# Kernel tuning notes

Hardware: AMD Instinct MI355X
Metric: run time of the kernel (lower is better)

The kernel has to match this reference:

```python
import jax, jax.numpy as jnp
import numpy as np

DIM = 1024
N_HEADS = 16
HEAD_DIM = DIM // N_HEADS


def setup_inputs() -> dict:
    key = jax.random.key(0)
    ks = jax.random.split(key, 5)
    s = 0.02
    return {
        "x": jax.random.normal(ks[0], (2, 2048, DIM), dtype=jnp.float32),
        "w_qkv": jax.random.normal(ks[1], (DIM, 3 * DIM), dtype=jnp.float32) * s,
        "b_qkv": jnp.zeros((3 * DIM,), dtype=jnp.float32),
        "w_proj": jax.random.normal(ks[2], (DIM, DIM), dtype=jnp.float32) * s,
        "b_proj": jnp.zeros((DIM,), dtype=jnp.float32),
    }


def reference(x, w_qkv, b_qkv, w_proj, b_proj):
    B, N, C = x.shape
    H, D = N_HEADS, HEAD_DIM
    qkv = x @ w_qkv + b_qkv                      # [B, N, 3C]
    qkv = qkv.reshape(B, N, 3, H, D)
    q = qkv[:, :, 0].transpose(0, 2, 1, 3)       # [B, H, N, D]
    k = qkv[:, :, 1].transpose(0, 2, 1, 3)
    v = qkv[:, :, 2].transpose(0, 2, 1, 3)
    scale = 1.0 / np.sqrt(D).astype(np.float32)
    attn = jnp.einsum('bhnd,bhmd->bhnm', q, k) * scale
    attn = jax.nn.softmax(attn, axis=-1)
    out = jnp.einsum('bhnm,bhmd->bhnd', attn, v)  # [B, H, N, D]
    out = out.transpose(0, 2, 1, 3).reshape(B, N, C)
    return out @ w_proj + b_proj
```

## Files before the change

### kernel.cpp

```cpp
#include <hip/hip_runtime.h>

#define DIM    1024
#define NHEADS 16
#define HDIM   64
#define BATCH  2
#define SEQ    2048
#define ROWS   (BATCH * SEQ)
#define KDIM   1024

typedef __attribute__((ext_vector_type(4))) float f32x4;
typedef __attribute__((ext_vector_type(16))) float f32x16;
typedef __attribute__((ext_vector_type(8))) short bf16x8;

__device__ inline unsigned short f2bf(float f) {
  return (unsigned short)((__float_as_uint(f) + 0x8000u) >> 16);
}
__device__ inline float bf2f(unsigned short h) {
  return __uint_as_float(((unsigned int)h) << 16);
}
__device__ inline void split2(float x, unsigned short& hi, unsigned short& lo) {
  hi = f2bf(x);
  lo = f2bf(x - bf2f(hi));
}
__device__ inline int key2(int r) { return (r & 3) ^ ((r >> 2) & 3); }
__device__ inline int key8(int r) { return (r & 7) ^ ((r >> 3) & 7); }

__device__ inline void gll16(const void* g, void* lds_base) {
  __builtin_amdgcn_global_load_lds(
      (const __attribute__((address_space(1))) void*)g,
      (__attribute__((address_space(3))) void*)lds_base, 16, 0, 0);
}
__device__ inline unsigned int cvtpk_bf16(float a, float b) {
  unsigned int r;
  asm("v_cvt_pk_bf16_f32 %0, %1, %2" : "=v"(r) : "v"(a), "v"(b));
  return r;
}

__global__ __launch_bounds__(256) void split_x_kernel(
    const float* __restrict__ x, ushort* __restrict__ Xh,
    ushort* __restrict__ Xl) {
  const int i = blockIdx.x * 256 + threadIdx.x;
  const float4 v = ((const float4*)x)[i];
  ushort4 h4, l4;
  split2(v.x, h4.x, l4.x);
  split2(v.y, h4.y, l4.y);
  split2(v.z, h4.z, l4.z);
  split2(v.w, h4.w, l4.w);
  ((ushort4*)Xh)[i] = h4;
  ((ushort4*)Xl)[i] = l4;
}

template <int Ndim, bool LO>
__global__ __launch_bounds__(256) void tsplit_w(const float* __restrict__ W,
                                                ushort* __restrict__ WTh,
                                                ushort* __restrict__ WTl) {
  __shared__ float Ls[64][68];
  const int t = threadIdx.x;
  const int n0 = blockIdx.x * 64, k0 = blockIdx.y * 64;
#pragma unroll
  for (int pass = 0; pass < 4; ++pass) {
    const int kk = pass * 16 + (t >> 4);
    const float4 v =
        *(const float4*)(W + (size_t)(k0 + kk) * Ndim + n0 + (t & 15) * 4);
    *(float4*)&Ls[kk][(t & 15) * 4] = v;
  }
  __syncthreads();
  const int nloc = t >> 2, kc = (t & 3) * 16;
#pragma unroll
  for (int j = 0; j < 4; ++j) {
    ushort4 h4, l4;
    split2(Ls[kc + j * 4 + 0][nloc], h4.x, l4.x);
    split2(Ls[kc + j * 4 + 1][nloc], h4.y, l4.y);
    split2(Ls[kc + j * 4 + 2][nloc], h4.z, l4.z);
    split2(Ls[kc + j * 4 + 3][nloc], h4.w, l4.w);
    const size_t off = (size_t)(n0 + nloc) * KDIM + k0 + kc + j * 4;
    *(ushort4*)(WTh + off) = h4;
    if (LO) *(ushort4*)(WTl + off) = l4;
  }
}

template <int NPROD, int MODE>
__global__ __launch_bounds__(256) void gemm_mfma(
    const ushort* __restrict__ Ahp, const ushort* __restrict__ Alp,
    const ushort* __restrict__ Bhp, const ushort* __restrict__ Blp,
    const float* __restrict__ bias, float* __restrict__ Cout,
    ushort* __restrict__ Qh, ushort* __restrict__ Kh,
    ushort* __restrict__ VTh, int Ndim) {
  constexpr int NPLANES = (NPROD == 3) ? 4 : 3;
  constexpr int CALLS = NPLANES * 512 / 256;
  __shared__ ushort lds[2][NPLANES * 128 * 32];

  const int t = threadIdx.x, w = t >> 6, lane = t & 63;
  const int l15 = lane & 15, lg = lane >> 4;
  const int n0 = blockIdx.x * 128, m0 = blockIdx.y * 128;
  const int wr = (w >> 1) * 64;
  const int wc = (w & 1) * 64;

  const ushort* srcs[4];
  srcs[0] = Ahp + (size_t)m0 * KDIM;
  srcs[1] = Alp + (size_t)m0 * KDIM;
  srcs[2] = Bhp + (size_t)n0 * KDIM;
  srcs[3] = (NPROD == 3) ? (Blp + (size_t)n0 * KDIM) : Bhp;

  f32x4 acc[4][4];
#pragma unroll
  for (int a = 0; a < 4; ++a)
#pragma unroll
    for (int bq = 0; bq < 4; ++bq) acc[a][bq] = (f32x4){0.f, 0.f, 0.f, 0.f};

  auto stage = [&](int bi, int k0) {
#pragma unroll
    for (int i = 0; i < CALLS; ++i) {
      const int cbase = (w * CALLS + i) * 64;
      const int c = cbase + lane;
      const int p = c >> 9, cc = c & 511, r = cc >> 2, s = cc & 3;
      const ushort* g = srcs[p] + (size_t)r * KDIM + k0 + ((s ^ key2(r)) << 3);
      gll16(g, (char*)&lds[bi][0] + cbase * 16);
    }
  };

  stage(0, 0);
  __syncthreads();

  for (int k0 = 0, it = 0; k0 < KDIM; k0 += 32, ++it) {
    const int cur = it & 1;
    if (k0 + 32 < KDIM) stage(cur ^ 1, k0 + 32);
    const ushort* L = &lds[cur][0];

    bf16x8 af[4][2];
#pragma unroll
    for (int mt = 0; mt < 4; ++mt) {
      const int row = wr + mt * 16 + l15;
      const int off = row * 32 + ((lg ^ key2(row)) << 3);
      af[mt][0] = *(const bf16x8*)&L[off];
      af[mt][1] = *(const bf16x8*)&L[4096 + off];
    }
#pragma unroll
    for (int nt = 0; nt < 4; ++nt) {
      const int row = wc + nt * 16 + l15;
      const int off = row * 32 + ((lg ^ key2(row)) << 3);
      const bf16x8 bh_ = *(const bf16x8*)&L[8192 + off];
#pragma unroll
      for (int mt = 0; mt < 4; ++mt) {
        acc[mt][nt] = __builtin_amdgcn_mfma_f32_16x16x32_bf16(
            af[mt][0], bh_, acc[mt][nt], 0, 0, 0);
        acc[mt][nt] = __builtin_amdgcn_mfma_f32_16x16x32_bf16(
            af[mt][1], bh_, acc[mt][nt], 0, 0, 0);
      }
      if constexpr (NPROD == 3) {
        const bf16x8 bl_ = *(const bf16x8*)&L[12288 + off];
#pragma unroll
        for (int mt = 0; mt < 4; ++mt)
          acc[mt][nt] = __builtin_amdgcn_mfma_f32_16x16x32_bf16(
              af[mt][0], bl_, acc[mt][nt], 0, 0, 0);
      }
    }
    __syncthreads();
  }

  if constexpr (MODE == 0) {
#pragma unroll
    for (int nt = 0; nt < 4; ++nt) {
      const int col = n0 + wc + nt * 16 + l15;
      const float bv = bias[col];
#pragma unroll
      for (int mt = 0; mt < 4; ++mt) {
        const int row = m0 + wr + mt * 16 + lg * 4;
#pragma unroll
        for (int r = 0; r < 4; ++r)
          Cout[(size_t)(row + r) * Ndim + col] = acc[mt][nt][r] + bv;
      }
    }
  } else {
    const int sec = n0 >> 10;
#pragma unroll
    for (int nt = 0; nt < 4; ++nt) {
      const int col = n0 + wc + nt * 16 + l15;
      const float bv = bias[col];
      const int cw = col & 1023;
      if (sec == 0) {
#pragma unroll
        for (int mt = 0; mt < 4; ++mt) {
          const int row = m0 + wr + mt * 16 + lg * 4;
#pragma unroll
          for (int r = 0; r < 4; ++r)
            Qh[(size_t)(row + r) * DIM + cw] =
                f2bf((acc[mt][nt][r] + bv) * 0.125f);
        }
      } else if (sec == 1) {
#pragma unroll
        for (int mt = 0; mt < 4; ++mt) {
          const int row = m0 + wr + mt * 16 + lg * 4;
#pragma unroll
          for (int r = 0; r < 4; ++r)
            Kh[(size_t)(row + r) * DIM + cw] = f2bf(acc[mt][nt][r] + bv);
        }
      } else {
        const int h = cw >> 6, d = cw & 63;
#pragma unroll
        for (int mt = 0; mt < 4; ++mt) {
          const int grow = m0 + wr + mt * 16 + lg * 4;
          const int b = grow >> 11, n = grow & 2047;
          ushort4 v4;
          v4.x = f2bf(acc[mt][nt][0] + bv);
          v4.y = f2bf(acc[mt][nt][1] + bv);
          v4.z = f2bf(acc[mt][nt][2] + bv);
          v4.w = f2bf(acc[mt][nt][3] + bv);
          *(ushort4*)(VTh + ((size_t)(b * NHEADS + h) * HDIM + d) * SEQ + n) =
              v4;
        }
      }
    }
  }
}

__global__ __launch_bounds__(256) void attn_mfma32(
    const ushort* __restrict__ Qhp, const ushort* __restrict__ Khp,
    const ushort* __restrict__ VThp, ushort* __restrict__ AOh,
    ushort* __restrict__ AOl) {
  __shared__ ushort KV2[2][2 * 64 * 64];

  const int t = threadIdx.x, w = t >> 6, lane = t & 63;
  const int l31 = lane & 31, hi = lane >> 5;
  const int q0 = blockIdx.x * 128;
  const int bh = blockIdx.y, b = bh >> 4, h = bh & 15;

  bf16x8 qf[4];
  {
    const ushort* qp = Qhp +
        (size_t)(b * SEQ + q0 + w * 32 + l31) * DIM + h * HDIM + hi * 8;
#pragma unroll
    for (int j = 0; j < 4; ++j) qf[j] = *(const bf16x8*)(qp + 16 * j);
  }
  const ushort* kbase = Khp + (size_t)(b * SEQ) * DIM + h * HDIM;
  const ushort* vbase = VThp + (size_t)(b * NHEADS + h) * HDIM * SEQ;

  float l_lane = 0.f;
  f32x16 o_[2];
  o_[0] = f32x16{};
  o_[1] = f32x16{};

  auto stage = [&](int bi, int kt) {
    const int kv0 = kt * 64;
#pragma unroll
    for (int i = 0; i < 4; ++i) {
      const int cbase = (w * 4 + i) * 64;
      const int c = cbase + lane;
      const int p_ = c >> 9, cc = c & 511, r = cc >> 3, s = cc & 7;
      const ushort* g =
          (p_ == 0)
              ? kbase + (size_t)(kv0 + r) * DIM + ((s ^ key8(r)) << 3)
              : vbase + (size_t)r * SEQ + kv0 + ((s ^ key8(r)) << 3);
      gll16(g, (char*)&KV2[bi][0] + cbase * 16);
    }
  };

  constexpr int NT = SEQ / 64;
  stage(0, 0);
  __syncthreads();

  for (int kt = 0; kt < NT; ++kt) {
    const int cur = kt & 1;
    if (kt + 1 < NT) stage(cur ^ 1, kt + 1);

    const ushort* Kt = &KV2[cur][0];
    const ushort* Vt = &KV2[cur][4096];

    f32x16 st[2];
    st[0] = f32x16{};
    st[1] = f32x16{};
#pragma unroll
    for (int j = 0; j < 4; ++j) {
#pragma unroll
      for (int rb = 0; rb < 2; ++rb) {
        const int n = rb * 32 + l31;
        const bf16x8 kf =
            *(const bf16x8*)&Kt[n * 64 + (((2 * j + hi) ^ key8(n)) << 3)];
        st[rb] = __builtin_amdgcn_mfma_f32_32x32x16_bf16(kf, qf[j], st[rb],
                                                         0, 0, 0);
      }
    }

    unsigned int u[2][8];
#pragma unroll
    for (int rb = 0; rb < 2; ++rb) {
      float p[16];
#pragma unroll
      for (int r = 0; r < 16; ++r) {
        p[r] = __expf(st[rb][r]);
        l_lane += p[r];
      }
#pragma unroll
      for (int j = 0; j < 8; ++j) u[rb][j] = cvtpk_bf16(p[2 * j], p[2 * j + 1]);
    }

#pragma unroll
    for (int kc = 0; kc < 4; ++kc) {
      bf16x8 pa;
      {
        const unsigned int* ub = &u[kc >> 1][4 * (kc & 1)];
        unsigned int tmp[4] = {ub[0], ub[1], ub[2], ub[3]};
        pa = *(const bf16x8*)tmp;
      }
#pragma unroll
      for (int dblk = 0; dblk < 2; ++dblk) {
        const int d = dblk * 32 + l31;
        const int rowoff = d * 64;
        const ushort4 va = *(const ushort4*)&Vt[rowoff +
            (((2 * kc) ^ key8(d)) << 3) + 4 * hi];
        const ushort4 vb = *(const ushort4*)&Vt[rowoff +
            (((2 * kc + 1) ^ key8(d)) << 3) + 4 * hi];
        ushort tmp[8] = {va.x, va.y, va.z, va.w, vb.x, vb.y, vb.z, vb.w};
        const bf16x8 vf = *(const bf16x8*)tmp;
        o_[dblk] = __builtin_amdgcn_mfma_f32_32x32x16_bf16(pa, vf, o_[dblk],
                                                           0, 0, 0);
      }
    }
    __syncthreads();
  }

  l_lane += __shfl_xor(l_lane, 32);

  float inv[16];
#pragma unroll
  for (int r = 0; r < 16; ++r) {
    const int ql = (r & 3) + 8 * (r >> 2) + 4 * hi;
    inv[r] = 1.0f / __shfl(l_lane, ql);
  }

#pragma unroll
  for (int dblk = 0; dblk < 2; ++dblk)
#pragma unroll
    for (int r = 0; r < 16; ++r) {
      const int q = q0 + w * 32 + (r & 3) + 8 * (r >> 2) + 4 * hi;
      unsigned short hi16, lo16;
      split2(o_[dblk][r] * inv[r], hi16, lo16);
      const size_t off =
          (size_t)(b * SEQ + q) * DIM + h * HDIM + dblk * 32 + l31;
      AOh[off] = hi16;
      AOl[off] = lo16;
    }
}

extern "C" void kernel_launch(void* const* d_in, const int* in_sizes, int n_in,
                              void* d_out, int out_size, void* d_ws,
                              size_t ws_size, hipStream_t stream) {
  const float* x      = (const float*)d_in[0];
  const float* w_qkv  = (const float*)d_in[1];
  const float* b_qkv  = (const float*)d_in[2];
  const float* w_proj = (const float*)d_in[3];
  const float* b_proj = (const float*)d_in[4];
  float* out = (float*)d_out;

  ushort* p = (ushort*)d_ws;
  ushort* WqT_h = p;  p += (size_t)3072 * 1024;
  ushort* WpT_h = p;  p += (size_t)1024 * 1024;
  ushort* WpT_l = p;  p += (size_t)1024 * 1024;
  ushort* Xh    = p;  p += (size_t)ROWS * 1024;
  ushort* Xl    = p;  p += (size_t)ROWS * 1024;
  ushort* Qh    = p;  p += (size_t)ROWS * 1024;
  ushort* Kh    = p;  p += (size_t)ROWS * 1024;
  ushort* VTh   = p;  p += (size_t)ROWS * 1024;
  ushort* AOh = Xh;
  ushort* AOl = Xl;

  split_x_kernel<<<ROWS * DIM / 4 / 256, 256, 0, stream>>>(x, Xh, Xl);
  tsplit_w<3072, false>
      <<<dim3(48, 16), 256, 0, stream>>>(w_qkv, WqT_h, nullptr);
  tsplit_w<1024, true>
      <<<dim3(16, 16), 256, 0, stream>>>(w_proj, WpT_h, WpT_l);

  gemm_mfma<2, 1><<<dim3(24, 32), 256, 0, stream>>>(
      Xh, Xl, WqT_h, nullptr, b_qkv, nullptr, Qh, Kh, VTh, 3072);

  attn_mfma32<<<dim3(SEQ / 128, BATCH * NHEADS), 256, 0, stream>>>(
      Qh, Kh, VTh, AOh, AOl);

  gemm_mfma<3, 0><<<dim3(8, 32), 256, 0, stream>>>(
      AOh, AOl, WpT_h, WpT_l, b_proj, out, nullptr, nullptr, nullptr, 1024);
}
```

Before: 161.4 us.

## Triple-buffer LDS staging in QKV GEMM and attention with vmcnt-based waits

Moves the QKV GEMM and the attention kernel from double to triple LDS buffering. Each iteration now waits on a partial vmcnt count and issues one raw barrier instead of a full __syncthreads at both ends, so global-to-LDS loads run two tiles ahead of compute. It also raises wave priority around the MFMA sections and forces the Q register loads to complete early. The cost is more LDS per block, which may lower occupancy, and correctness now depends on the hand-coded vmcnt values matching the number of loads issued per stage.

```diff
diff --git a/kernel.cpp b/kernel.cpp
--- a/kernel.cpp
+++ b/kernel.cpp
@@ -34,6 +34,13 @@
   unsigned int r;
   asm("v_cvt_pk_bf16_f32 %0, %1, %2" : "=v"(r) : "v"(a), "v"(b));
   return r;
+}
+template <int N>
+__device__ inline void vm_wait() {
+  if constexpr (N == 0)      asm volatile("s_waitcnt vmcnt(0)" ::: "memory");
+  else if constexpr (N == 4) asm volatile("s_waitcnt vmcnt(4)" ::: "memory");
+  else if constexpr (N == 6) asm volatile("s_waitcnt vmcnt(6)" ::: "memory");
+  else                       asm volatile("s_waitcnt vmcnt(8)" ::: "memory");
 }
 
 __global__ __launch_bounds__(256) void split_x_kernel(
@@ -79,7 +86,7 @@
   }
 }
 
-template <int NPROD, int MODE>
+template <int NPROD, int MODE, bool PIPE3>
 __global__ __launch_bounds__(256) void gemm_mfma(
     const ushort* __restrict__ Ahp, const ushort* __restrict__ Alp,
     const ushort* __restrict__ Bhp, const ushort* __restrict__ Blp,
@@ -87,8 +94,10 @@
     ushort* __restrict__ Qh, ushort* __restrict__ Kh,
     ushort* __restrict__ VTh, int Ndim) {
   constexpr int NPLANES = (NPROD == 3) ? 4 : 3;
-  constexpr int CALLS = NPLANES * 512 / 256;
-  __shared__ ushort lds[2][NPLANES * 128 * 32];
+  constexpr int CALLS = NPLANES * 2;
+  constexpr int BUFE = NPLANES * 128 * 32;
+  constexpr int NBUF = PIPE3 ? 3 : 2;
+  __shared__ ushort lds[NBUF][BUFE];
 
   const int t = threadIdx.x, w = t >> 6, lane = t & 63;
   const int l15 = lane & 15, lg = lane >> 4;
@@ -119,14 +128,7 @@
     }
   };
 
-  stage(0, 0);
-  __syncthreads();
-
-  for (int k0 = 0, it = 0; k0 < KDIM; k0 += 32, ++it) {
-    const int cur = it & 1;
-    if (k0 + 32 < KDIM) stage(cur ^ 1, k0 + 32);
-    const ushort* L = &lds[cur][0];
-
+  auto compute = [&](const ushort* L) {
     bf16x8 af[4][2];
 #pragma unroll
     for (int mt = 0; mt < 4; ++mt) {
@@ -135,6 +137,7 @@
       af[mt][0] = *(const bf16x8*)&L[off];
       af[mt][1] = *(const bf16x8*)&L[4096 + off];
     }
+    __builtin_amdgcn_s_setprio(1);
 #pragma unroll
     for (int nt = 0; nt < 4; ++nt) {
       const int row = wc + nt * 16 + l15;
@@ -155,7 +158,29 @@
               af[mt][0], bl_, acc[mt][nt], 0, 0, 0);
       }
     }
+    __builtin_amdgcn_s_setprio(0);
+  };
+
+  if constexpr (PIPE3) {
+    constexpr int NSTEP = KDIM / 32;
+    stage(0, 0);
+    stage(1, 32);
+    for (int it = 0; it < NSTEP; ++it) {
+      if (it + 1 < NSTEP) vm_wait<CALLS>(); else vm_wait<0>();
+      __builtin_amdgcn_s_barrier();
+      __builtin_amdgcn_sched_barrier(0);
+      if (it + 2 < NSTEP) stage((it + 2) % 3, (it + 2) * 32);
+      compute(&lds[it % 3][0]);
+    }
+  } else {
+    stage(0, 0);
     __syncthreads();
+    for (int k0 = 0, it = 0; k0 < KDIM; k0 += 32, ++it) {
+      const int cur = it & 1;
+      if (k0 + 32 < KDIM) stage(cur ^ 1, k0 + 32);
+      compute(&lds[cur][0]);
+      __syncthreads();
+    }
   }
 
   if constexpr (MODE == 0) {
@@ -218,7 +243,7 @@
     const ushort* __restrict__ Qhp, const ushort* __restrict__ Khp,
     const ushort* __restrict__ VThp, ushort* __restrict__ AOh,
     ushort* __restrict__ AOl) {
-  __shared__ ushort KV2[2][2 * 64 * 64];
+  __shared__ ushort KV2[3][2 * 64 * 64];
 
   const int t = threadIdx.x, w = t >> 6, lane = t & 63;
   const int l31 = lane & 31, hi = lane >> 5;
@@ -229,8 +254,15 @@
   {
     const ushort* qp = Qhp +
         (size_t)(b * SEQ + q0 + w * 32 + l31) * DIM + h * HDIM + hi * 8;
-#pragma unroll
-    for (int j = 0; j < 4; ++j) qf[j] = *(const bf16x8*)(qp + 16 * j);
+    int4 qi[4];
+#pragma unroll
+    for (int j = 0; j < 4; ++j) qi[j] = *(const int4*)(qp + 16 * j);
+#pragma unroll
+    for (int j = 0; j < 4; ++j) {
+      asm volatile("" :: "v"(qi[j].x), "v"(qi[j].y), "v"(qi[j].z),
+                   "v"(qi[j].w));
+      qf[j] = __builtin_bit_cast(bf16x8, qi[j]);
+    }
   }
   const ushort* kbase = Khp + (size_t)(b * SEQ) * DIM + h * HDIM;
   const ushort* vbase = VThp + (size_t)(b * NHEADS + h) * HDIM * SEQ;
@@ -257,18 +289,21 @@
 
   constexpr int NT = SEQ / 64;
   stage(0, 0);
-  __syncthreads();
+  stage(1, 1);
 
   for (int kt = 0; kt < NT; ++kt) {
-    const int cur = kt & 1;
-    if (kt + 1 < NT) stage(cur ^ 1, kt + 1);
-
-    const ushort* Kt = &KV2[cur][0];
-    const ushort* Vt = &KV2[cur][4096];
+    if (kt + 1 < NT) vm_wait<4>(); else vm_wait<0>();
+    __builtin_amdgcn_s_barrier();
+    __builtin_amdgcn_sched_barrier(0);
+    if (kt + 2 < NT) stage((kt + 2) % 3, kt + 2);
+
+    const ushort* Kt = &KV2[kt % 3][0];
+    const ushort* Vt = &KV2[kt % 3][4096];
 
     f32x16 st[2];
     st[0] = f32x16{};
     st[1] = f32x16{};
+    __builtin_amdgcn_s_setprio(1);
 #pragma unroll
     for (int j = 0; j < 4; ++j) {
 #pragma unroll
@@ -280,6 +315,7 @@
                                                          0, 0, 0);
       }
     }
+    __builtin_amdgcn_s_setprio(0);
 
     unsigned int u[2][8];
 #pragma unroll
@@ -294,6 +330,7 @@
       for (int j = 0; j < 8; ++j) u[rb][j] = cvtpk_bf16(p[2 * j], p[2 * j + 1]);
     }
 
+    __builtin_amdgcn_s_setprio(1);
 #pragma unroll
     for (int kc = 0; kc < 4; ++kc) {
       bf16x8 pa;
@@ -316,7 +353,7 @@
                                                            0, 0, 0);
       }
     }
-    __syncthreads();
+    __builtin_amdgcn_s_setprio(0);
   }
 
   l_lane += __shfl_xor(l_lane, 32);
@@ -370,12 +407,12 @@
   tsplit_w<1024, true>
       <<<dim3(16, 16), 256, 0, stream>>>(w_proj, WpT_h, WpT_l);
 
-  gemm_mfma<2, 1><<<dim3(24, 32), 256, 0, stream>>>(
+  gemm_mfma<2, 1, true><<<dim3(24, 32), 256, 0, stream>>>(
       Xh, Xl, WqT_h, nullptr, b_qkv, nullptr, Qh, Kh, VTh, 3072);
 
   attn_mfma32<<<dim3(SEQ / 128, BATCH * NHEADS), 256, 0, stream>>>(
       Qh, Kh, VTh, AOh, AOl);
 
-  gemm_mfma<3, 0><<<dim3(8, 32), 256, 0, stream>>>(
+  gemm_mfma<3, 0, false><<<dim3(8, 32), 256, 0, stream>>>(
       AOh, AOl, WpT_h, WpT_l, b_proj, out, nullptr, nullptr, nullptr, 1024);
 }
```

New measurement: 164.9 us. 1.02x slower.
